# Kernel optimization log

Hardware: AMD Instinct MI355X
Metric: run time of the kernel (lower is better)

The kernel has to match this reference:

```python
import jax, jax.numpy as jnp
import numpy as np

MSL, BS, ENC = 64, 128, 1024
HID, EMB, ATOM = 512, 50, 64
MAX_STEPS = 50
SOS = 1


def setup_inputs() -> dict:
    key = jax.random.key(0)
    ks = jax.random.split(key, 14)
    s = 0.05
    emb = jax.random.normal(ks[1], (ATOM, EMB), jnp.float32) * s
    emb = emb.at[0].set(0.0)  # padding_idx=0
    return {
        'encoder_output': jax.random.normal(ks[0], (MSL, BS, ENC), jnp.float32),
        'emb': emb,
        'w_h0': jax.random.normal(ks[2], (2 * HID, ENC), jnp.float32) * s,
        'b_h0': jax.random.normal(ks[3], (2 * HID,), jnp.float32) * s,
        'w_ih0': jax.random.normal(ks[4], (3 * HID, EMB), jnp.float32) * s,
        'w_hh0': jax.random.normal(ks[5], (3 * HID, HID), jnp.float32) * s,
        'b_ih0': jax.random.normal(ks[6], (3 * HID,), jnp.float32) * s,
        'b_hh0': jax.random.normal(ks[7], (3 * HID,), jnp.float32) * s,
        'w_ih1': jax.random.normal(ks[8], (3 * HID, HID), jnp.float32) * s,
        'w_hh1': jax.random.normal(ks[9], (3 * HID, HID), jnp.float32) * s,
        'b_ih1': jax.random.normal(ks[10], (3 * HID,), jnp.float32) * s,
        'b_hh1': jax.random.normal(ks[11], (3 * HID,), jnp.float32) * s,
        'w_out': jax.random.normal(ks[12], (ATOM, HID), jnp.float32) * s,
        'b_out': jax.random.normal(ks[13], (ATOM,), jnp.float32) * s,
    }


def _gru_cell(x, h, w_ih, w_hh, b_ih, b_hh):
    gi = x @ w_ih.T + b_ih          # [B, 3H]
    gh = h @ w_hh.T + b_hh          # [B, 3H]
    i_r, i_z, i_n = jnp.split(gi, 3, axis=-1)
    h_r, h_z, h_n = jnp.split(gh, 3, axis=-1)
    r = jax.nn.sigmoid(i_r + h_r)
    z = jax.nn.sigmoid(i_z + h_z)
    n = jnp.tanh(i_n + r * h_n)
    return (1.0 - z) * n + z * h


def reference(encoder_output, emb, w_h0, b_h0, w_ih0, w_hh0, b_ih0, b_hh0,
              w_ih1, w_hh1, b_ih1, b_hh1, w_out, b_out):
    msl, bs, _ = encoder_output.shape
    B = msl * bs
    H = w_hh0.shape[1]
    # encoder_to_h0: Linear + Tanh -> [B, 2, H] -> [2, B, H]
    h = jnp.tanh(encoder_output.reshape(B, -1) @ w_h0.T + b_h0)
    h = h.reshape(B, 2, H).transpose(1, 0, 2)
    h0, h1 = h[0], h[1]
    e = jnp.broadcast_to(emb[SOS], (B, emb.shape[1]))  # SOS embedding

    def step(carry, _):
        h0, h1, e = carry
        h0 = _gru_cell(e, h0, w_ih0, w_hh0, b_ih0, b_hh0)
        h1 = _gru_cell(h0, h1, w_ih1, w_hh1, b_ih1, b_hh1)
        y = jax.nn.log_softmax(h1 @ w_out.T + b_out, axis=-1)  # [B, A]
        p = jnp.argmax(y, axis=-1)
        e = emb[p]
        return (h0, h1, e), y

    _, Y = jax.lax.scan(step, (h0, h1, e), None, length=MAX_STEPS)
    return Y.reshape(MAX_STEPS, msl, bs, -1)[:-1]
```

## Files before the change

kernel.cpp:

```cpp
#include <hip/hip_runtime.h>
#include <hip/hip_bf16.h>
#include <cstdint>
#include <cstddef>


typedef __attribute__((ext_vector_type(8))) __bf16 bf16x8;
typedef __attribute__((ext_vector_type(4))) __bf16 bf16x4;
typedef __attribute__((ext_vector_type(4))) float f32x4;

#define B_ROWS 8192
#define HID 512
#define GATE3 1536
#define ATOM 64
#define NSTEP 49

#define GLOAD_LDS16(gp, sp)                                                   \
  __builtin_amdgcn_global_load_lds(                                           \
      (__attribute__((address_space(1))) void*)(gp),                          \
      (__attribute__((address_space(3))) void*)(sp), 16, 0, 0)

#define PROLOGUE_FENCE()                                                      \
  do {                                                                        \
    __builtin_amdgcn_sched_barrier(0);                                        \
    asm volatile("" ::: "memory");                                            \
  } while (0)

#define BARRIER_FENCED()                                                      \
  do {                                                                        \
    __builtin_amdgcn_s_barrier();                                             \
    asm volatile("" ::: "memory");                                            \
    __builtin_amdgcn_sched_barrier(0);                                        \
  } while (0)

__device__ inline float sig_(float x) { return 1.f / (1.f + __expf(-x)); }
__device__ inline float tanh_(float x) { return 2.f / (1.f + __expf(-2.f * x)) - 1.f; }

__global__ __launch_bounds__(256) void gru0_step(
    const __bf16* __restrict__ h0b_c, const __bf16* __restrict__ whh0f,
    const float* __restrict__ G0p, const int* __restrict__ p,
    const float* __restrict__ bhh0p,
    const float* __restrict__ h0f_c, float* __restrict__ h0f_n,
    __bf16* __restrict__ h0b_n)
{
    __shared__ __bf16 As[3][64 * 32];

    const int tid = threadIdx.x, lane = tid & 63, w = tid >> 6;
    const int u = lane & 15, q = lane >> 4;
    const int m0 = blockIdx.x * 64;
    const int t_ = blockIdx.y * 4 + w;
    const int j  = t_ * 16 + u;
    const int qb = t_ * 48 + u;
    const int k0   = (q ^ ((u >> 1) & 3)) * 8;
    const int scol = ((tid & 3) ^ ((tid >> 3) & 3)) * 8;
    const int wo = w * 512;

    const __bf16* Ap = h0b_c + (size_t)(m0 + (tid >> 2)) * HID + scol;
    const __bf16* Bf = whh0f + (size_t)(t_ * 48) * 512 + lane * 8;
    #define BFR0(g, kt) (*(const bf16x8*)(Bf + (size_t)((g) * 16 + (kt)) * 512))

    f32x4 acc[4][3] = {};
    bf16x8 bfr[2][3];

    GLOAD_LDS16(Ap, &As[0][wo]); Ap += 32;
    bfr[0][0] = BFR0(0, 0);
    bfr[0][1] = BFR0(1, 0);
    bfr[0][2] = BFR0(2, 0);
    PROLOGUE_FENCE();

    #pragma unroll
    for (int kt = 0; kt < 16; ++kt) {
        const int cur3 = kt % 3, nxt3 = (kt + 1) % 3;
        const int cur2 = kt & 1;
        if (kt < 15) {
            GLOAD_LDS16(Ap, &As[nxt3][wo]); Ap += 32;
            bfr[cur2 ^ 1][0] = BFR0(0, kt + 1);
            bfr[cur2 ^ 1][1] = BFR0(1, kt + 1);
            bfr[cur2 ^ 1][2] = BFR0(2, kt + 1);
            if (kt == 0) asm volatile("s_waitcnt vmcnt(0)" ::: "memory");
            else         asm volatile("s_waitcnt vmcnt(4)" ::: "memory");
        } else {
            asm volatile("s_waitcnt vmcnt(0)" ::: "memory");
        }
        BARRIER_FENCED();

        bf16x8 af[4];
        #pragma unroll
        for (int mf = 0; mf < 4; ++mf)
            af[mf] = *(const bf16x8*)&As[cur3][(mf * 16 + u) * 32 + k0];
        __builtin_amdgcn_s_setprio(1);
        #pragma unroll
        for (int mf = 0; mf < 4; ++mf)
            #pragma unroll
            for (int g = 0; g < 3; ++g)
                acc[mf][g] = __builtin_amdgcn_mfma_f32_16x16x32_bf16(
                    af[mf], bfr[cur2][g], acc[mf][g], 0, 0, 0);
        __builtin_amdgcn_s_setprio(0);
    }

    const float bhr = bhh0p[qb], bhz = bhh0p[qb + 16], bhn = bhh0p[qb + 32];
    const int rbase = m0 + (q << 2);
    #pragma unroll
    for (int mf = 0; mf < 4; ++mf)
        #pragma unroll
        for (int r = 0; r < 4; ++r) {
            const int row = rbase + mf * 16 + r;
            const float* g0 = G0p + (size_t)p[row] * GATE3 + qb;
            const float rr = sig_(g0[0]  + acc[mf][0][r] + bhr);
            const float zz = sig_(g0[16] + acc[mf][1][r] + bhz);
            const float nn = tanh_(g0[32] + rr * (acc[mf][2][r] + bhn));
            const float hp = h0f_c[(size_t)row * HID + j];
            const float hv = (1.f - zz) * nn + zz * hp;
            h0f_n[(size_t)row * HID + j] = hv;
            h0b_n[(size_t)row * HID + j] = (__bf16)hv;
        }
}

__global__ __launch_bounds__(256) void gru1_fused(
    const __bf16* __restrict__ h0b_n, const __bf16* __restrict__ wih1f,
    const __bf16* __restrict__ h1b_c, const __bf16* __restrict__ whh1f,
    const float* __restrict__ bih1p, const float* __restrict__ bhh1p,
    const float* __restrict__ h1f_c, float* __restrict__ h1f_n,
    __bf16* __restrict__ h1b_n)
{
    __shared__ __bf16 Asi[3][64 * 32];
    __shared__ __bf16 Ash[3][64 * 32];

    const int tid = threadIdx.x, lane = tid & 63, w = tid >> 6;
    const int u = lane & 15, q = lane >> 4;
    const int m0 = blockIdx.x * 64;
    const int t_ = blockIdx.y * 4 + w;
    const int j  = t_ * 16 + u;
    const int qb = t_ * 48 + u;
    const int k0   = (q ^ ((u >> 1) & 3)) * 8;
    const int scol = ((tid & 3) ^ ((tid >> 3) & 3)) * 8;
    const int wo = w * 512;

    const __bf16* Api = h0b_n + (size_t)(m0 + (tid >> 2)) * HID + scol;
    const __bf16* Aph = h1b_c + (size_t)(m0 + (tid >> 2)) * HID + scol;
    const __bf16* Bfi = wih1f + (size_t)(t_ * 48) * 512 + lane * 8;
    const __bf16* Bfh = whh1f + (size_t)(t_ * 48) * 512 + lane * 8;
    #define BFRI(g, kt) (*(const bf16x8*)(Bfi + (size_t)((g) * 16 + (kt)) * 512))
    #define BFRH(g, kt) (*(const bf16x8*)(Bfh + (size_t)((g) * 16 + (kt)) * 512))

    f32x4 acc_i[4][3] = {};
    f32x4 acc_h[4][3] = {};
    bf16x8 bfi[2][3], bfh[2][3];

    GLOAD_LDS16(Api, &Asi[0][wo]); Api += 32;
    GLOAD_LDS16(Aph, &Ash[0][wo]); Aph += 32;
    #pragma unroll
    for (int g = 0; g < 3; ++g) {
        bfi[0][g] = BFRI(g, 0);
        bfh[0][g] = BFRH(g, 0);
    }
    PROLOGUE_FENCE();

    #pragma unroll
    for (int kt = 0; kt < 16; ++kt) {
        const int cur3 = kt % 3, nxt3 = (kt + 1) % 3;
        const int cur2 = kt & 1;
        if (kt < 15) {
            GLOAD_LDS16(Api, &Asi[nxt3][wo]); Api += 32;
            GLOAD_LDS16(Aph, &Ash[nxt3][wo]); Aph += 32;
            #pragma unroll
            for (int g = 0; g < 3; ++g) {
                bfi[cur2 ^ 1][g] = BFRI(g, kt + 1);
                bfh[cur2 ^ 1][g] = BFRH(g, kt + 1);
            }
            if (kt == 0) asm volatile("s_waitcnt vmcnt(0)" ::: "memory");
            else         asm volatile("s_waitcnt vmcnt(8)" ::: "memory");
        } else {
            asm volatile("s_waitcnt vmcnt(0)" ::: "memory");
        }
        BARRIER_FENCED();

        #pragma unroll
        for (int mf = 0; mf < 4; ++mf) {
            const bf16x8 afi = *(const bf16x8*)&Asi[cur3][(mf * 16 + u) * 32 + k0];
            const bf16x8 afh = *(const bf16x8*)&Ash[cur3][(mf * 16 + u) * 32 + k0];
            __builtin_amdgcn_s_setprio(1);
            #pragma unroll
            for (int g = 0; g < 3; ++g)
                acc_i[mf][g] = __builtin_amdgcn_mfma_f32_16x16x32_bf16(
                    afi, bfi[cur2][g], acc_i[mf][g], 0, 0, 0);
            #pragma unroll
            for (int g = 0; g < 3; ++g)
                acc_h[mf][g] = __builtin_amdgcn_mfma_f32_16x16x32_bf16(
                    afh, bfh[cur2][g], acc_h[mf][g], 0, 0, 0);
            __builtin_amdgcn_s_setprio(0);
        }
    }

    const float bir = bih1p[qb], biz = bih1p[qb + 16], bin = bih1p[qb + 32];
    const float bhr = bhh1p[qb], bhz = bhh1p[qb + 16], bhn = bhh1p[qb + 32];
    const int rbase = m0 + (q << 2);
    #pragma unroll
    for (int mf = 0; mf < 4; ++mf)
        #pragma unroll
        for (int r = 0; r < 4; ++r) {
            const int row = rbase + mf * 16 + r;
            const float rr = sig_(acc_i[mf][0][r] + bir + acc_h[mf][0][r] + bhr);
            const float zz = sig_(acc_i[mf][1][r] + biz + acc_h[mf][1][r] + bhz);
            const float nn = tanh_(acc_i[mf][2][r] + bin +
                                   rr * (acc_h[mf][2][r] + bhn));
            const float hp = h1f_c[(size_t)row * HID + j];
            const float hv = (1.f - zz) * nn + zz * hp;
            h1f_n[(size_t)row * HID + j] = hv;
            h1b_n[(size_t)row * HID + j] = (__bf16)hv;
        }
}

__global__ __launch_bounds__(128) void out_mfma(
    const __bf16* __restrict__ h1b, const __bf16* __restrict__ woutf,
    const float* __restrict__ bout, float* __restrict__ y, int* __restrict__ p)
{
    __shared__ __bf16 As[3][32 * 32];

    const int tid  = threadIdx.x;
    const int lane = tid & 63;
    const int w    = tid >> 6;
    const int m0   = blockIdx.x * 32;
    const int u    = lane & 15, q = lane >> 4;
    const int k0   = (q ^ ((u >> 1) & 3)) * 8;
    const int scol = ((tid & 3) ^ ((tid >> 3) & 3)) * 8;
    const int wo   = w * 512;

    f32x4 acc[4] = {};
    bf16x8 bfr[2][4];

    const __bf16* Ap = h1b + (size_t)(m0 + (tid >> 2)) * HID + scol;
    const __bf16* Bf = woutf + lane * 8;
    #define BFRW(nf, kt) (*(const bf16x8*)(Bf + (size_t)((nf) * 16 + (kt)) * 512))

    GLOAD_LDS16(Ap, &As[0][wo]); Ap += 32;
    #pragma unroll
    for (int nf = 0; nf < 4; ++nf) bfr[0][nf] = BFRW(nf, 0);
    PROLOGUE_FENCE();

    #pragma unroll
    for (int kt = 0; kt < 16; ++kt) {
        const int cur3 = kt % 3, nxt3 = (kt + 1) % 3;
        const int cur2 = kt & 1;
        if (kt < 15) {
            GLOAD_LDS16(Ap, &As[nxt3][wo]); Ap += 32;
            #pragma unroll
            for (int nf = 0; nf < 4; ++nf) bfr[cur2 ^ 1][nf] = BFRW(nf, kt + 1);
            if (kt == 0) asm volatile("s_waitcnt vmcnt(0)" ::: "memory");
            else         asm volatile("s_waitcnt vmcnt(5)" ::: "memory");
        } else {
            asm volatile("s_waitcnt vmcnt(0)" ::: "memory");
        }
        BARRIER_FENCED();

        const bf16x8 af = *(const bf16x8*)&As[cur3][(w * 16 + u) * 32 + k0];
        __builtin_amdgcn_s_setprio(1);
        #pragma unroll
        for (int nf = 0; nf < 4; ++nf)
            acc[nf] = __builtin_amdgcn_mfma_f32_16x16x32_bf16(
                af, bfr[cur2][nf], acc[nf], 0, 0, 0);
        __builtin_amdgcn_s_setprio(0);
    }

    #pragma unroll
    for (int r = 0; r < 4; ++r) {
        const int row = m0 + w * 16 + (q << 2) + r;
        float l[4];
        #pragma unroll
        for (int nf = 0; nf < 4; ++nf) l[nf] = acc[nf][r] + bout[nf * 16 + u];

        float mv = l[0]; int mi = u;
        #pragma unroll
        for (int nf = 1; nf < 4; ++nf)
            if (l[nf] > mv) { mv = l[nf]; mi = nf * 16 + u; }
        #pragma unroll
        for (int off = 1; off <= 8; off <<= 1) {
            const float ov = __shfl_xor(mv, off, 64);
            const int   oi = __shfl_xor(mi, off, 64);
            if (ov > mv || (ov == mv && oi < mi)) { mv = ov; mi = oi; }
        }
        float se = 0.f;
        #pragma unroll
        for (int nf = 0; nf < 4; ++nf) se += __expf(l[nf] - mv);
        #pragma unroll
        for (int off = 1; off <= 8; off <<= 1) se += __shfl_xor(se, off, 64);
        const float lse = logf(se);

        #pragma unroll
        for (int nf = 0; nf < 4; ++nf)
            y[(size_t)row * ATOM + nf * 16 + u] = l[nf] - mv - lse;
        if (u == 0) p[row] = mi;
    }
}

__global__ __launch_bounds__(256) void gemm_init(
    const __bf16* __restrict__ A, const __bf16* __restrict__ B,
    int N, int K, const float* __restrict__ bias,
    float* __restrict__ H0f, __bf16* __restrict__ H0b,
    float* __restrict__ H1f, __bf16* __restrict__ H1b)
{
    __shared__ __bf16 As[128 * 32];
    __shared__ __bf16 Bs[128 * 32];

    const int tid  = threadIdx.x;
    const int lane = tid & 63;
    const int w    = tid >> 6;
    const int wm   = w >> 1, wn = w & 1;
    const int m0   = blockIdx.x * 128;
    const int n0   = blockIdx.y * 128;

    f32x4 acc[4][4] = {};

    const int i0 = w * 64 + lane;
    const int i1 = i0 + 256;
    const __bf16* Ap0 = A + (size_t)(m0 + (i0 >> 2)) * K + (i0 & 3) * 8;
    const __bf16* Ap1 = A + (size_t)(m0 + (i1 >> 2)) * K + (i1 & 3) * 8;
    const __bf16* Bp0 = B + (size_t)(n0 + (i0 >> 2)) * K + (i0 & 3) * 8;
    const __bf16* Bp1 = B + (size_t)(n0 + (i1 >> 2)) * K + (i1 & 3) * 8;
    __bf16* As0 = As + w * 512;
    __bf16* As1 = As + 2048 + w * 512;
    __bf16* Bs0 = Bs + w * 512;
    __bf16* Bs1 = Bs + 2048 + w * 512;

    const int mrow = wm * 64 + (lane & 15);
    const int nrow = wn * 64 + (lane & 15);
    const int koff = (lane >> 4) * 8;

    for (int kt = 0; kt < K / 32; ++kt) {
        __syncthreads();
        GLOAD_LDS16(Ap0, As0);
        GLOAD_LDS16(Ap1, As1);
        GLOAD_LDS16(Bp0, Bs0);
        GLOAD_LDS16(Bp1, Bs1);
        Ap0 += 32; Ap1 += 32; Bp0 += 32; Bp1 += 32;
        __syncthreads();

        bf16x8 af[4], bfr[4];
        #pragma unroll
        for (int f = 0; f < 4; ++f) {
            af[f]  = *(const bf16x8*)&As[(mrow + f * 16) * 32 + koff];
            bfr[f] = *(const bf16x8*)&Bs[(nrow + f * 16) * 32 + koff];
        }
        #pragma unroll
        for (int mf = 0; mf < 4; ++mf)
            #pragma unroll
            for (int nf = 0; nf < 4; ++nf)
                acc[mf][nf] = __builtin_amdgcn_mfma_f32_16x16x32_bf16(
                    af[mf], bfr[nf], acc[mf][nf], 0, 0, 0);
    }

    const int colb = n0 + wn * 64 + (lane & 15);
    const int rowb = m0 + wm * 64 + ((lane >> 4) << 2);
    #pragma unroll
    for (int mf = 0; mf < 4; ++mf)
        #pragma unroll
        for (int nf = 0; nf < 4; ++nf) {
            const int col = colb + nf * 16;
            #pragma unroll
            for (int r = 0; r < 4; ++r) {
                const int row = rowb + mf * 16 + r;
                const float v = tanhf(acc[mf][nf][r] + bias[col]);
                if (col < HID) {
                    H0f[(size_t)row * HID + col] = v;
                    H0b[(size_t)row * HID + col] = (__bf16)v;
                } else {
                    H1f[(size_t)row * HID + col - HID] = v;
                    H1b[(size_t)row * HID + col - HID] = (__bf16)v;
                }
            }
        }
}

__device__ inline int permQ(int q) {
    const int t = q / 48, rem = q % 48;
    return (rem / 16) * HID + t * 16 + (rem % 16);
}

__device__ inline size_t fragOff(int r, int k) {
    return (size_t)((r >> 4) * 16 + (k >> 5)) * 512 +
           ((k >> 3) & 3) * 128 + (r & 15) * 8 + (k & 7);
}

__global__ __launch_bounds__(256) void f2b(const float* __restrict__ s,
                                           __bf16* __restrict__ d, int n)
{
    const int i = (blockIdx.x * 256 + threadIdx.x) * 4;
    if (i + 3 < n) {
        const float4 v = *(const float4*)(s + i);
        bf16x4 o = { (__bf16)v.x, (__bf16)v.y, (__bf16)v.z, (__bf16)v.w };
        *(bf16x4*)(d + i) = o;
    }
}

__global__ __launch_bounds__(256) void f2bpf(const float* __restrict__ s,
                                             __bf16* __restrict__ d)
{
    const int idx = blockIdx.x * 256 + threadIdx.x;
    const int q = idx >> 7, k4 = (idx & 127) << 2;
    const int o = permQ(q);
    const float4 v = *(const float4*)(s + (size_t)o * HID + k4);
    bf16x4 ov = { (__bf16)v.x, (__bf16)v.y, (__bf16)v.z, (__bf16)v.w };
    *(bf16x4*)(d + fragOff(q, k4)) = ov;
}

__global__ __launch_bounds__(256) void f2bf(const float* __restrict__ s,
                                            __bf16* __restrict__ d)
{
    const int idx = blockIdx.x * 256 + threadIdx.x;
    if (idx >= ATOM * 128) return;
    const int r = idx >> 7, k4 = (idx & 127) << 2;
    const float4 v = *(const float4*)(s + (size_t)r * HID + k4);
    bf16x4 ov = { (__bf16)v.x, (__bf16)v.y, (__bf16)v.z, (__bf16)v.w };
    *(bf16x4*)(d + fragOff(r, k4)) = ov;
}

__global__ __launch_bounds__(256) void bperm(const float* __restrict__ s,
                                             float* __restrict__ d)
{
    const int q = blockIdx.x * 256 + threadIdx.x;
    if (q < GATE3) d[q] = s[permQ(q)];
}

__global__ __launch_bounds__(256) void g0pk(const float* __restrict__ emb,
                                            const float* __restrict__ wih0,
                                            const float* __restrict__ bih0,
                                            float* __restrict__ G0p)
{
    const int i = blockIdx.x * 256 + threadIdx.x;
    if (i >= ATOM * GATE3) return;
    const int a = i / GATE3, q = i % GATE3;
    const int o = permQ(q);
    float s = bih0[o];
    for (int k = 0; k < 50; ++k) s += emb[a * 50 + k] * wih0[o * 50 + k];
    G0p[i] = s;
}

__global__ __launch_bounds__(256) void initp(int* __restrict__ p)
{
    const int i = blockIdx.x * 256 + threadIdx.x;
    if (i < B_ROWS) p[i] = 1;
}

extern "C" void kernel_launch(void* const* d_in, const int* in_sizes, int n_in,
                              void* d_out, int out_size, void* d_ws, size_t ws_size,
                              hipStream_t stream)
{
    (void)in_sizes; (void)n_in; (void)out_size; (void)ws_size;
    const float* enc   = (const float*)d_in[0];
    const float* emb   = (const float*)d_in[1];
    const float* w_h0  = (const float*)d_in[2];
    const float* b_h0  = (const float*)d_in[3];
    const float* w_ih0 = (const float*)d_in[4];
    const float* w_hh0 = (const float*)d_in[5];
    const float* b_ih0 = (const float*)d_in[6];
    const float* b_hh0 = (const float*)d_in[7];
    const float* w_ih1 = (const float*)d_in[8];
    const float* w_hh1 = (const float*)d_in[9];
    const float* b_ih1 = (const float*)d_in[10];
    const float* b_hh1 = (const float*)d_in[11];
    const float* w_out = (const float*)d_in[12];
    const float* b_out = (const float*)d_in[13];
    float* out = (float*)d_out;

    char* ws = (char*)d_ws;
    size_t off = 0;
    auto alloc = [&](size_t bytes) -> void* {
        void* pp = ws + off;
        off = (off + bytes + 255) & ~(size_t)255;
        return pp;
    };
    __bf16* whh0f = (__bf16*)alloc((size_t)GATE3 * HID * 2);
    __bf16* wih1f = (__bf16*)alloc((size_t)GATE3 * HID * 2);
    __bf16* whh1f = (__bf16*)alloc((size_t)GATE3 * HID * 2);
    __bf16* woutf = (__bf16*)alloc((size_t)ATOM * HID * 2);
    float*  G0p   = (float*) alloc((size_t)ATOM * GATE3 * 4);
    float*  bhh0p = (float*) alloc(GATE3 * 4);
    float*  bih1p = (float*) alloc(GATE3 * 4);
    float*  bhh1p = (float*) alloc(GATE3 * 4);
    float*  h0f[2]; __bf16* h0b[2]; float* h1f[2]; __bf16* h1b[2];
    for (int i = 0; i < 2; ++i) {
        h0f[i] = (float*) alloc((size_t)B_ROWS * HID * 4);
        h0b[i] = (__bf16*)alloc((size_t)B_ROWS * HID * 2);
        h1f[i] = (float*) alloc((size_t)B_ROWS * HID * 4);
        h1b[i] = (__bf16*)alloc((size_t)B_ROWS * HID * 2);
    }
    int* p = (int*)alloc((size_t)B_ROWS * 4);
    __bf16* enc_b = (__bf16*)alloc((size_t)B_ROWS * 1024 * 2);
    __bf16* wh0b  = (__bf16*)alloc((size_t)1024 * 1024 * 2);

    f2b  <<<8192, 256, 0, stream>>>(enc,  enc_b, B_ROWS * 1024);
    f2b  <<<1024, 256, 0, stream>>>(w_h0, wh0b,  1024 * 1024);
    f2bf <<<32,   256, 0, stream>>>(w_out, woutf);
    f2bpf<<<768,  256, 0, stream>>>(w_hh0, whh0f);
    f2bpf<<<768,  256, 0, stream>>>(w_ih1, wih1f);
    f2bpf<<<768,  256, 0, stream>>>(w_hh1, whh1f);
    bperm<<<6, 256, 0, stream>>>(b_hh0, bhh0p);
    bperm<<<6, 256, 0, stream>>>(b_ih1, bih1p);
    bperm<<<6, 256, 0, stream>>>(b_hh1, bhh1p);
    g0pk<<<384, 256, 0, stream>>>(emb, w_ih0, b_ih0, G0p);
    initp<<<32, 256, 0, stream>>>(p);

    gemm_init<<<dim3(B_ROWS / 128, 1024 / 128), 256, 0, stream>>>(
        enc_b, wh0b, 1024, 1024, b_h0, h0f[0], h0b[0], h1f[0], h1b[0]);

    const dim3 gGrid(B_ROWS / 64, GATE3 / 192);
    for (int step = 0; step < NSTEP; ++step) {
        const int cur = step & 1, nxt = cur ^ 1;
        gru0_step<<<gGrid, 256, 0, stream>>>(
            h0b[cur], whh0f, G0p, p, bhh0p, h0f[cur], h0f[nxt], h0b[nxt]);
        gru1_fused<<<gGrid, 256, 0, stream>>>(
            h0b[nxt], wih1f, h1b[cur], whh1f, bih1p, bhh1p,
            h1f[cur], h1f[nxt], h1b[nxt]);
        out_mfma<<<B_ROWS / 32, 128, 0, stream>>>(
            h1b[nxt], woutf, b_out, out + (size_t)step * B_ROWS * ATOM, p);
    }
}
```

Baseline: 3.898 ms.

## Double GRU row tile to 128 and merge gru1 r/z accumulation over concatenated K

Both GRU step kernels now process 128 rows per block instead of 64, so each weight fragment loaded from global memory is reused across twice as many MFMAs and the grid halves. In gru1_fused, the input and hidden GEMMs are treated as one K=1024 loop over a shared LDS buffer: the r and z gates accumulate into a single accumulator, and only the n gate keeps separate input and hidden accumulators. This cuts accumulator registers and MFMA count for r/z, at the cost of a longer serial K loop, more registers per wave for the wider M tile, and fewer blocks to fill the GPU.

```diff
diff --git a/kernel.cpp b/kernel.cpp
--- a/kernel.cpp
+++ b/kernel.cpp
@@ -42,11 +42,11 @@
     const float* __restrict__ h0f_c, float* __restrict__ h0f_n,
     __bf16* __restrict__ h0b_n)
 {
-    __shared__ __bf16 As[3][64 * 32];
+    __shared__ __bf16 As[3][128 * 32];
 
     const int tid = threadIdx.x, lane = tid & 63, w = tid >> 6;
     const int u = lane & 15, q = lane >> 4;
-    const int m0 = blockIdx.x * 64;
+    const int m0 = blockIdx.x * 128;
     const int t_ = blockIdx.y * 4 + w;
     const int j  = t_ * 16 + u;
     const int qb = t_ * 48 + u;
@@ -54,14 +54,17 @@
     const int scol = ((tid & 3) ^ ((tid >> 3) & 3)) * 8;
     const int wo = w * 512;
 
-    const __bf16* Ap = h0b_c + (size_t)(m0 + (tid >> 2)) * HID + scol;
+    const __bf16* Ap0 = h0b_c + (size_t)(m0 + (tid >> 2)) * HID + scol;
+    const __bf16* Ap1 = Ap0 + (size_t)64 * HID;
     const __bf16* Bf = whh0f + (size_t)(t_ * 48) * 512 + lane * 8;
     #define BFR0(g, kt) (*(const bf16x8*)(Bf + (size_t)((g) * 16 + (kt)) * 512))
 
-    f32x4 acc[4][3] = {};
+    f32x4 acc[8][3] = {};
     bf16x8 bfr[2][3];
 
-    GLOAD_LDS16(Ap, &As[0][wo]); Ap += 32;
+    GLOAD_LDS16(Ap0, &As[0][wo]);
+    GLOAD_LDS16(Ap1, &As[0][2048 + wo]);
+    Ap0 += 32; Ap1 += 32;
     bfr[0][0] = BFR0(0, 0);
     bfr[0][1] = BFR0(1, 0);
     bfr[0][2] = BFR0(2, 0);
@@ -72,24 +75,26 @@
         const int cur3 = kt % 3, nxt3 = (kt + 1) % 3;
         const int cur2 = kt & 1;
         if (kt < 15) {
-            GLOAD_LDS16(Ap, &As[nxt3][wo]); Ap += 32;
+            GLOAD_LDS16(Ap0, &As[nxt3][wo]);
+            GLOAD_LDS16(Ap1, &As[nxt3][2048 + wo]);
+            Ap0 += 32; Ap1 += 32;
             bfr[cur2 ^ 1][0] = BFR0(0, kt + 1);
             bfr[cur2 ^ 1][1] = BFR0(1, kt + 1);
             bfr[cur2 ^ 1][2] = BFR0(2, kt + 1);
             if (kt == 0) asm volatile("s_waitcnt vmcnt(0)" ::: "memory");
-            else         asm volatile("s_waitcnt vmcnt(4)" ::: "memory");
+            else         asm volatile("s_waitcnt vmcnt(5)" ::: "memory");
         } else {
             asm volatile("s_waitcnt vmcnt(0)" ::: "memory");
         }
         BARRIER_FENCED();
 
-        bf16x8 af[4];
-        #pragma unroll
-        for (int mf = 0; mf < 4; ++mf)
+        bf16x8 af[8];
+        #pragma unroll
+        for (int mf = 0; mf < 8; ++mf)
             af[mf] = *(const bf16x8*)&As[cur3][(mf * 16 + u) * 32 + k0];
         __builtin_amdgcn_s_setprio(1);
         #pragma unroll
-        for (int mf = 0; mf < 4; ++mf)
+        for (int mf = 0; mf < 8; ++mf)
             #pragma unroll
             for (int g = 0; g < 3; ++g)
                 acc[mf][g] = __builtin_amdgcn_mfma_f32_16x16x32_bf16(
@@ -100,7 +105,7 @@
     const float bhr = bhh0p[qb], bhz = bhh0p[qb + 16], bhn = bhh0p[qb + 32];
     const int rbase = m0 + (q << 2);
     #pragma unroll
-    for (int mf = 0; mf < 4; ++mf)
+    for (int mf = 0; mf < 8; ++mf)
         #pragma unroll
         for (int r = 0; r < 4; ++r) {
             const int row = rbase + mf * 16 + r;
@@ -122,12 +127,11 @@
     const float* __restrict__ h1f_c, float* __restrict__ h1f_n,
     __bf16* __restrict__ h1b_n)
 {
-    __shared__ __bf16 Asi[3][64 * 32];
-    __shared__ __bf16 Ash[3][64 * 32];
+    __shared__ __bf16 As[3][128 * 32];
 
     const int tid = threadIdx.x, lane = tid & 63, w = tid >> 6;
     const int u = lane & 15, q = lane >> 4;
-    const int m0 = blockIdx.x * 64;
+    const int m0 = blockIdx.x * 128;
     const int t_ = blockIdx.y * 4 + w;
     const int j  = t_ * 16 + u;
     const int qb = t_ * 48 + u;
@@ -135,74 +139,80 @@
     const int scol = ((tid & 3) ^ ((tid >> 3) & 3)) * 8;
     const int wo = w * 512;
 
-    const __bf16* Api = h0b_n + (size_t)(m0 + (tid >> 2)) * HID + scol;
-    const __bf16* Aph = h1b_c + (size_t)(m0 + (tid >> 2)) * HID + scol;
-    const __bf16* Bfi = wih1f + (size_t)(t_ * 48) * 512 + lane * 8;
-    const __bf16* Bfh = whh1f + (size_t)(t_ * 48) * 512 + lane * 8;
-    #define BFRI(g, kt) (*(const bf16x8*)(Bfi + (size_t)((g) * 16 + (kt)) * 512))
-    #define BFRH(g, kt) (*(const bf16x8*)(Bfh + (size_t)((g) * 16 + (kt)) * 512))
-
-    f32x4 acc_i[4][3] = {};
-    f32x4 acc_h[4][3] = {};
-    bf16x8 bfi[2][3], bfh[2][3];
-
-    GLOAD_LDS16(Api, &Asi[0][wo]); Api += 32;
-    GLOAD_LDS16(Aph, &Ash[0][wo]); Aph += 32;
-    #pragma unroll
-    for (int g = 0; g < 3; ++g) {
-        bfi[0][g] = BFRI(g, 0);
-        bfh[0][g] = BFRH(g, 0);
-    }
+    const __bf16* Ai0 = h0b_n + (size_t)(m0 + (tid >> 2)) * HID + scol;
+    const __bf16* Ai1 = Ai0 + (size_t)64 * HID;
+    const __bf16* Ah0 = h1b_c + (size_t)(m0 + (tid >> 2)) * HID + scol;
+    const __bf16* Ah1 = Ah0 + (size_t)64 * HID;
+    const __bf16* Bi = wih1f + (size_t)(t_ * 48) * 512 + lane * 8;
+    const __bf16* Bh = whh1f + (size_t)(t_ * 48) * 512 + lane * 8;
+
+    f32x4 arz[8][2] = {};
+    f32x4 ani[8] = {};
+    f32x4 anh[8] = {};
+    bf16x8 bfr[2][3];
+
+    GLOAD_LDS16(Ai0, &As[0][wo]);
+    GLOAD_LDS16(Ai1, &As[0][2048 + wo]);
+    #pragma unroll
+    for (int g = 0; g < 3; ++g)
+        bfr[0][g] = *(const bf16x8*)(Bi + (size_t)(g * 16) * 512);
     PROLOGUE_FENCE();
 
     #pragma unroll
-    for (int kt = 0; kt < 16; ++kt) {
+    for (int kt = 0; kt < 32; ++kt) {
         const int cur3 = kt % 3, nxt3 = (kt + 1) % 3;
         const int cur2 = kt & 1;
-        if (kt < 15) {
-            GLOAD_LDS16(Api, &Asi[nxt3][wo]); Api += 32;
-            GLOAD_LDS16(Aph, &Ash[nxt3][wo]); Aph += 32;
+        if (kt < 31) {
+            const int kn = kt + 1;
+            const __bf16* a0 = (kn < 16 ? Ai0 : Ah0) + (size_t)(kn & 15) * 32;
+            const __bf16* a1 = (kn < 16 ? Ai1 : Ah1) + (size_t)(kn & 15) * 32;
+            GLOAD_LDS16(a0, &As[nxt3][wo]);
+            GLOAD_LDS16(a1, &As[nxt3][2048 + wo]);
+            const __bf16* bb = (kn < 16 ? Bi : Bh);
             #pragma unroll
-            for (int g = 0; g < 3; ++g) {
-                bfi[cur2 ^ 1][g] = BFRI(g, kt + 1);
-                bfh[cur2 ^ 1][g] = BFRH(g, kt + 1);
-            }
+            for (int g = 0; g < 3; ++g)
+                bfr[cur2 ^ 1][g] = *(const bf16x8*)(bb + (size_t)(g * 16 + (kn & 15)) * 512);
             if (kt == 0) asm volatile("s_waitcnt vmcnt(0)" ::: "memory");
-            else         asm volatile("s_waitcnt vmcnt(8)" ::: "memory");
+            else         asm volatile("s_waitcnt vmcnt(5)" ::: "memory");
         } else {
             asm volatile("s_waitcnt vmcnt(0)" ::: "memory");
         }
         BARRIER_FENCED();
 
-        #pragma unroll
-        for (int mf = 0; mf < 4; ++mf) {
-            const bf16x8 afi = *(const bf16x8*)&Asi[cur3][(mf * 16 + u) * 32 + k0];
-            const bf16x8 afh = *(const bf16x8*)&Ash[cur3][(mf * 16 + u) * 32 + k0];
-            __builtin_amdgcn_s_setprio(1);
-            #pragma unroll
-            for (int g = 0; g < 3; ++g)
-                acc_i[mf][g] = __builtin_amdgcn_mfma_f32_16x16x32_bf16(
-                    afi, bfi[cur2][g], acc_i[mf][g], 0, 0, 0);
-            #pragma unroll
-            for (int g = 0; g < 3; ++g)
-                acc_h[mf][g] = __builtin_amdgcn_mfma_f32_16x16x32_bf16(
-                    afh, bfh[cur2][g], acc_h[mf][g], 0, 0, 0);
-            __builtin_amdgcn_s_setprio(0);
-        }
-    }
-
-    const float bir = bih1p[qb], biz = bih1p[qb + 16], bin = bih1p[qb + 32];
-    const float bhr = bhh1p[qb], bhz = bhh1p[qb + 16], bhn = bhh1p[qb + 32];
+        bf16x8 af[8];
+        #pragma unroll
+        for (int mf = 0; mf < 8; ++mf)
+            af[mf] = *(const bf16x8*)&As[cur3][(mf * 16 + u) * 32 + k0];
+        __builtin_amdgcn_s_setprio(1);
+        #pragma unroll
+        for (int mf = 0; mf < 8; ++mf) {
+            arz[mf][0] = __builtin_amdgcn_mfma_f32_16x16x32_bf16(
+                af[mf], bfr[cur2][0], arz[mf][0], 0, 0, 0);
+            arz[mf][1] = __builtin_amdgcn_mfma_f32_16x16x32_bf16(
+                af[mf], bfr[cur2][1], arz[mf][1], 0, 0, 0);
+            if (kt < 16)
+                ani[mf] = __builtin_amdgcn_mfma_f32_16x16x32_bf16(
+                    af[mf], bfr[cur2][2], ani[mf], 0, 0, 0);
+            else
+                anh[mf] = __builtin_amdgcn_mfma_f32_16x16x32_bf16(
+                    af[mf], bfr[cur2][2], anh[mf], 0, 0, 0);
+        }
+        __builtin_amdgcn_s_setprio(0);
+    }
+
+    const float b1r  = bih1p[qb] + bhh1p[qb];
+    const float b1z  = bih1p[qb + 16] + bhh1p[qb + 16];
+    const float b1in = bih1p[qb + 32];
+    const float b1hn = bhh1p[qb + 32];
     const int rbase = m0 + (q << 2);
     #pragma unroll
-    for (int mf = 0; mf < 4; ++mf)
+    for (int mf = 0; mf < 8; ++mf)
         #pragma unroll
         for (int r = 0; r < 4; ++r) {
             const int row = rbase + mf * 16 + r;
-            const float rr = sig_(acc_i[mf][0][r] + bir + acc_h[mf][0][r] + bhr);
-            const float zz = sig_(acc_i[mf][1][r] + biz + acc_h[mf][1][r] + bhz);
-            const float nn = tanh_(acc_i[mf][2][r] + bin +
-                                   rr * (acc_h[mf][2][r] + bhn));
+            const float rr = sig_(arz[mf][0][r] + b1r);
+            const float zz = sig_(arz[mf][1][r] + b1z);
+            const float nn = tanh_(ani[mf][r] + b1in + rr * (anh[mf][r] + b1hn));
             const float hp = h1f_c[(size_t)row * HID + j];
             const float hv = (1.f - zz) * nn + zz * hp;
             h1f_n[(size_t)row * HID + j] = hv;
@@ -502,7 +512,7 @@
     gemm_init<<<dim3(B_ROWS / 128, 1024 / 128), 256, 0, stream>>>(
         enc_b, wh0b, 1024, 1024, b_h0, h0f[0], h0b[0], h1f[0], h1b[0]);
 
-    const dim3 gGrid(B_ROWS / 64, GATE3 / 192);
+    const dim3 gGrid(B_ROWS / 128, GATE3 / 192);
     for (int step = 0; step < NSTEP; ++step) {
         const int cur = step & 1, nxt = cur ^ 1;
         gru0_step<<<gGrid, 256, 0, stream>>>(
```

After: 5.448 ms. 39.8% more time.

## Deepen K-loop prefetch to three stages and merge GRU1 input/hidden GEMMs

Applied to the files above, without the earlier changes.

All three GEMM kernels move from a one-step-ahead prefetch to a 4-slot ring with three tiles in flight, with vmcnt waits adjusted to match. The barrier now comes before issuing the next loads, which allows fewer buffers per hazard. In gru1_fused the two separate input and hidden GEMMs become one 32-step K loop with shared LDS. The r and z gates accumulate into one accumulator and only the n gate is kept split, which cuts accumulator registers and LDS. The aim is to hide global load latency better, at the cost of more B-fragment registers in flight.

```diff
diff --git a/kernel.cpp b/kernel.cpp
--- a/kernel.cpp
+++ b/kernel.cpp
@@ -42,7 +42,7 @@
     const float* __restrict__ h0f_c, float* __restrict__ h0f_n,
     __bf16* __restrict__ h0b_n)
 {
-    __shared__ __bf16 As[3][64 * 32];
+    __shared__ __bf16 As[4][64 * 32];
 
     const int tid = threadIdx.x, lane = tid & 63, w = tid >> 6;
     const int u = lane & 15, q = lane >> 4;
@@ -59,41 +59,45 @@
     #define BFR0(g, kt) (*(const bf16x8*)(Bf + (size_t)((g) * 16 + (kt)) * 512))
 
     f32x4 acc[4][3] = {};
-    bf16x8 bfr[2][3];
-
-    GLOAD_LDS16(Ap, &As[0][wo]); Ap += 32;
-    bfr[0][0] = BFR0(0, 0);
-    bfr[0][1] = BFR0(1, 0);
-    bfr[0][2] = BFR0(2, 0);
-    PROLOGUE_FENCE();
+    bf16x8 bfr[4][3];
+
+    #pragma unroll
+    for (int pg = 0; pg < 3; ++pg) {
+        GLOAD_LDS16(Ap, &As[pg][wo]); Ap += 32;
+        bfr[pg][0] = BFR0(0, pg);
+        bfr[pg][1] = BFR0(1, pg);
+        bfr[pg][2] = BFR0(2, pg);
+        PROLOGUE_FENCE();
+    }
 
     #pragma unroll
     for (int kt = 0; kt < 16; ++kt) {
-        const int cur3 = kt % 3, nxt3 = (kt + 1) % 3;
-        const int cur2 = kt & 1;
-        if (kt < 15) {
-            GLOAD_LDS16(Ap, &As[nxt3][wo]); Ap += 32;
-            bfr[cur2 ^ 1][0] = BFR0(0, kt + 1);
-            bfr[cur2 ^ 1][1] = BFR0(1, kt + 1);
-            bfr[cur2 ^ 1][2] = BFR0(2, kt + 1);
-            if (kt == 0) asm volatile("s_waitcnt vmcnt(0)" ::: "memory");
-            else         asm volatile("s_waitcnt vmcnt(4)" ::: "memory");
-        } else {
-            asm volatile("s_waitcnt vmcnt(0)" ::: "memory");
-        }
+        if (kt == 0)       asm volatile("s_waitcnt vmcnt(0)" ::: "memory");
+        else if (kt <= 13) asm volatile("s_waitcnt vmcnt(8)" ::: "memory");
+        else if (kt == 14) asm volatile("s_waitcnt vmcnt(4)" ::: "memory");
+        else               asm volatile("s_waitcnt vmcnt(0)" ::: "memory");
         BARRIER_FENCED();
 
+        if (kt + 3 < 16) {
+            const int s = (kt + 3) & 3;
+            GLOAD_LDS16(Ap, &As[s][wo]); Ap += 32;
+            bfr[s][0] = BFR0(0, kt + 3);
+            bfr[s][1] = BFR0(1, kt + 3);
+            bfr[s][2] = BFR0(2, kt + 3);
+            PROLOGUE_FENCE();
+        }
+
         bf16x8 af[4];
         #pragma unroll
         for (int mf = 0; mf < 4; ++mf)
-            af[mf] = *(const bf16x8*)&As[cur3][(mf * 16 + u) * 32 + k0];
+            af[mf] = *(const bf16x8*)&As[kt & 3][(mf * 16 + u) * 32 + k0];
         __builtin_amdgcn_s_setprio(1);
         #pragma unroll
         for (int mf = 0; mf < 4; ++mf)
             #pragma unroll
             for (int g = 0; g < 3; ++g)
                 acc[mf][g] = __builtin_amdgcn_mfma_f32_16x16x32_bf16(
-                    af[mf], bfr[cur2][g], acc[mf][g], 0, 0, 0);
+                    af[mf], bfr[kt & 3][g], acc[mf][g], 0, 0, 0);
         __builtin_amdgcn_s_setprio(0);
     }
 
@@ -122,8 +126,7 @@
     const float* __restrict__ h1f_c, float* __restrict__ h1f_n,
     __bf16* __restrict__ h1b_n)
 {
-    __shared__ __bf16 Asi[3][64 * 32];
-    __shared__ __bf16 Ash[3][64 * 32];
+    __shared__ __bf16 As[4][64 * 32];
 
     const int tid = threadIdx.x, lane = tid & 63, w = tid >> 6;
     const int u = lane & 15, q = lane >> 4;
@@ -135,74 +138,78 @@
     const int scol = ((tid & 3) ^ ((tid >> 3) & 3)) * 8;
     const int wo = w * 512;
 
-    const __bf16* Api = h0b_n + (size_t)(m0 + (tid >> 2)) * HID + scol;
-    const __bf16* Aph = h1b_c + (size_t)(m0 + (tid >> 2)) * HID + scol;
-    const __bf16* Bfi = wih1f + (size_t)(t_ * 48) * 512 + lane * 8;
-    const __bf16* Bfh = whh1f + (size_t)(t_ * 48) * 512 + lane * 8;
-    #define BFRI(g, kt) (*(const bf16x8*)(Bfi + (size_t)((g) * 16 + (kt)) * 512))
-    #define BFRH(g, kt) (*(const bf16x8*)(Bfh + (size_t)((g) * 16 + (kt)) * 512))
-
-    f32x4 acc_i[4][3] = {};
-    f32x4 acc_h[4][3] = {};
-    bf16x8 bfi[2][3], bfh[2][3];
-
-    GLOAD_LDS16(Api, &Asi[0][wo]); Api += 32;
-    GLOAD_LDS16(Aph, &Ash[0][wo]); Aph += 32;
-    #pragma unroll
-    for (int g = 0; g < 3; ++g) {
-        bfi[0][g] = BFRI(g, 0);
-        bfh[0][g] = BFRH(g, 0);
-    }
-    PROLOGUE_FENCE();
-
-    #pragma unroll
-    for (int kt = 0; kt < 16; ++kt) {
-        const int cur3 = kt % 3, nxt3 = (kt + 1) % 3;
-        const int cur2 = kt & 1;
-        if (kt < 15) {
-            GLOAD_LDS16(Api, &Asi[nxt3][wo]); Api += 32;
-            GLOAD_LDS16(Aph, &Ash[nxt3][wo]); Aph += 32;
-            #pragma unroll
-            for (int g = 0; g < 3; ++g) {
-                bfi[cur2 ^ 1][g] = BFRI(g, kt + 1);
-                bfh[cur2 ^ 1][g] = BFRH(g, kt + 1);
-            }
-            if (kt == 0) asm volatile("s_waitcnt vmcnt(0)" ::: "memory");
-            else         asm volatile("s_waitcnt vmcnt(8)" ::: "memory");
-        } else {
-            asm volatile("s_waitcnt vmcnt(0)" ::: "memory");
-        }
+    const __bf16* Ai = h0b_n + (size_t)(m0 + (tid >> 2)) * HID + scol;
+    const __bf16* Ah = h1b_c + (size_t)(m0 + (tid >> 2)) * HID + scol;
+    const __bf16* Bi = wih1f + (size_t)(t_ * 48) * 512 + lane * 8;
+    const __bf16* Bh = whh1f + (size_t)(t_ * 48) * 512 + lane * 8;
+
+    f32x4 arz[4][2] = {};
+    f32x4 ani[4] = {};
+    f32x4 anh[4] = {};
+    bf16x8 bfr[4][3];
+
+    #pragma unroll
+    for (int pg = 0; pg < 3; ++pg) {
+        GLOAD_LDS16(Ai + (size_t)pg * 32, &As[pg][wo]);
+        bfr[pg][0] = *(const bf16x8*)(Bi + (size_t)(0 * 16 + pg) * 512);
+        bfr[pg][1] = *(const bf16x8*)(Bi + (size_t)(1 * 16 + pg) * 512);
+        bfr[pg][2] = *(const bf16x8*)(Bi + (size_t)(2 * 16 + pg) * 512);
+        PROLOGUE_FENCE();
+    }
+
+    #pragma unroll
+    for (int kt = 0; kt < 32; ++kt) {
+        if (kt == 0)       asm volatile("s_waitcnt vmcnt(0)" ::: "memory");
+        else if (kt <= 29) asm volatile("s_waitcnt vmcnt(8)" ::: "memory");
+        else if (kt == 30) asm volatile("s_waitcnt vmcnt(4)" ::: "memory");
+        else               asm volatile("s_waitcnt vmcnt(0)" ::: "memory");
         BARRIER_FENCED();
 
+        if (kt + 3 < 32) {
+            const int t = kt + 3, s = t & 3;
+            const __bf16* ap = (t < 16 ? Ai : Ah) + (size_t)(t & 15) * 32;
+            const __bf16* bp = (t < 16 ? Bi : Bh);
+            GLOAD_LDS16(ap, &As[s][wo]);
+            bfr[s][0] = *(const bf16x8*)(bp + (size_t)(0 * 16 + (t & 15)) * 512);
+            bfr[s][1] = *(const bf16x8*)(bp + (size_t)(1 * 16 + (t & 15)) * 512);
+            bfr[s][2] = *(const bf16x8*)(bp + (size_t)(2 * 16 + (t & 15)) * 512);
+            PROLOGUE_FENCE();
+        }
+
+        bf16x8 af[4];
+        #pragma unroll
+        for (int mf = 0; mf < 4; ++mf)
+            af[mf] = *(const bf16x8*)&As[kt & 3][(mf * 16 + u) * 32 + k0];
+        __builtin_amdgcn_s_setprio(1);
         #pragma unroll
         for (int mf = 0; mf < 4; ++mf) {
-            const bf16x8 afi = *(const bf16x8*)&Asi[cur3][(mf * 16 + u) * 32 + k0];
-            const bf16x8 afh = *(const bf16x8*)&Ash[cur3][(mf * 16 + u) * 32 + k0];
-            __builtin_amdgcn_s_setprio(1);
-            #pragma unroll
-            for (int g = 0; g < 3; ++g)
-                acc_i[mf][g] = __builtin_amdgcn_mfma_f32_16x16x32_bf16(
-                    afi, bfi[cur2][g], acc_i[mf][g], 0, 0, 0);
-            #pragma unroll
-            for (int g = 0; g < 3; ++g)
-                acc_h[mf][g] = __builtin_amdgcn_mfma_f32_16x16x32_bf16(
-                    afh, bfh[cur2][g], acc_h[mf][g], 0, 0, 0);
-            __builtin_amdgcn_s_setprio(0);
-        }
-    }
-
-    const float bir = bih1p[qb], biz = bih1p[qb + 16], bin = bih1p[qb + 32];
-    const float bhr = bhh1p[qb], bhz = bhh1p[qb + 16], bhn = bhh1p[qb + 32];
+            arz[mf][0] = __builtin_amdgcn_mfma_f32_16x16x32_bf16(
+                af[mf], bfr[kt & 3][0], arz[mf][0], 0, 0, 0);
+            arz[mf][1] = __builtin_amdgcn_mfma_f32_16x16x32_bf16(
+                af[mf], bfr[kt & 3][1], arz[mf][1], 0, 0, 0);
+            if (kt < 16)
+                ani[mf] = __builtin_amdgcn_mfma_f32_16x16x32_bf16(
+                    af[mf], bfr[kt & 3][2], ani[mf], 0, 0, 0);
+            else
+                anh[mf] = __builtin_amdgcn_mfma_f32_16x16x32_bf16(
+                    af[mf], bfr[kt & 3][2], anh[mf], 0, 0, 0);
+        }
+        __builtin_amdgcn_s_setprio(0);
+    }
+
+    const float b1r  = bih1p[qb] + bhh1p[qb];
+    const float b1z  = bih1p[qb + 16] + bhh1p[qb + 16];
+    const float b1in = bih1p[qb + 32];
+    const float b1hn = bhh1p[qb + 32];
     const int rbase = m0 + (q << 2);
     #pragma unroll
     for (int mf = 0; mf < 4; ++mf)
         #pragma unroll
         for (int r = 0; r < 4; ++r) {
             const int row = rbase + mf * 16 + r;
-            const float rr = sig_(acc_i[mf][0][r] + bir + acc_h[mf][0][r] + bhr);
-            const float zz = sig_(acc_i[mf][1][r] + biz + acc_h[mf][1][r] + bhz);
-            const float nn = tanh_(acc_i[mf][2][r] + bin +
-                                   rr * (acc_h[mf][2][r] + bhn));
+            const float rr = sig_(arz[mf][0][r] + b1r);
+            const float zz = sig_(arz[mf][1][r] + b1z);
+            const float nn = tanh_(ani[mf][r] + b1in + rr * (anh[mf][r] + b1hn));
             const float hp = h1f_c[(size_t)row * HID + j];
             const float hv = (1.f - zz) * nn + zz * hp;
             h1f_n[(size_t)row * HID + j] = hv;
@@ -214,7 +221,7 @@
     const __bf16* __restrict__ h1b, const __bf16* __restrict__ woutf,
     const float* __restrict__ bout, float* __restrict__ y, int* __restrict__ p)
 {
-    __shared__ __bf16 As[3][32 * 32];
+    __shared__ __bf16 As[4][32 * 32];
 
     const int tid  = threadIdx.x;
     const int lane = tid & 63;
@@ -226,38 +233,42 @@
     const int wo   = w * 512;
 
     f32x4 acc[4] = {};
-    bf16x8 bfr[2][4];
+    bf16x8 bfr[4][4];
 
     const __bf16* Ap = h1b + (size_t)(m0 + (tid >> 2)) * HID + scol;
     const __bf16* Bf = woutf + lane * 8;
     #define BFRW(nf, kt) (*(const bf16x8*)(Bf + (size_t)((nf) * 16 + (kt)) * 512))
 
-    GLOAD_LDS16(Ap, &As[0][wo]); Ap += 32;
-    #pragma unroll
-    for (int nf = 0; nf < 4; ++nf) bfr[0][nf] = BFRW(nf, 0);
-    PROLOGUE_FENCE();
+    #pragma unroll
+    for (int pg = 0; pg < 3; ++pg) {
+        GLOAD_LDS16(Ap, &As[pg][wo]); Ap += 32;
+        #pragma unroll
+        for (int nf = 0; nf < 4; ++nf) bfr[pg][nf] = BFRW(nf, pg);
+        PROLOGUE_FENCE();
+    }
 
     #pragma unroll
     for (int kt = 0; kt < 16; ++kt) {
-        const int cur3 = kt % 3, nxt3 = (kt + 1) % 3;
-        const int cur2 = kt & 1;
-        if (kt < 15) {
-            GLOAD_LDS16(Ap, &As[nxt3][wo]); Ap += 32;
+        if (kt == 0)       asm volatile("s_waitcnt vmcnt(0)" ::: "memory");
+        else if (kt <= 13) asm volatile("s_waitcnt vmcnt(10)" ::: "memory");
+        else if (kt == 14) asm volatile("s_waitcnt vmcnt(5)" ::: "memory");
+        else               asm volatile("s_waitcnt vmcnt(0)" ::: "memory");
+        BARRIER_FENCED();
+
+        if (kt + 3 < 16) {
+            const int s = (kt + 3) & 3;
+            GLOAD_LDS16(Ap, &As[s][wo]); Ap += 32;
             #pragma unroll
-            for (int nf = 0; nf < 4; ++nf) bfr[cur2 ^ 1][nf] = BFRW(nf, kt + 1);
-            if (kt == 0) asm volatile("s_waitcnt vmcnt(0)" ::: "memory");
-            else         asm volatile("s_waitcnt vmcnt(5)" ::: "memory");
-        } else {
-            asm volatile("s_waitcnt vmcnt(0)" ::: "memory");
-        }
-        BARRIER_FENCED();
-
-        const bf16x8 af = *(const bf16x8*)&As[cur3][(w * 16 + u) * 32 + k0];
+            for (int nf = 0; nf < 4; ++nf) bfr[s][nf] = BFRW(nf, kt + 3);
+            PROLOGUE_FENCE();
+        }
+
+        const bf16x8 af = *(const bf16x8*)&As[kt & 3][(w * 16 + u) * 32 + k0];
         __builtin_amdgcn_s_setprio(1);
         #pragma unroll
         for (int nf = 0; nf < 4; ++nf)
             acc[nf] = __builtin_amdgcn_mfma_f32_16x16x32_bf16(
-                af, bfr[cur2][nf], acc[nf], 0, 0, 0);
+                af, bfr[kt & 3][nf], acc[nf], 0, 0, 0);
         __builtin_amdgcn_s_setprio(0);
     }
 
```

Measured after the change: 3.512 ms. 1.11x faster.
